# Kernel optimization log

Hardware: AMD Instinct MI355X
Metric: run time of the kernel (lower is better)

The kernel has to match this reference:

```python
import jax, jax.numpy as jnp
import numpy as np

IN_C, DIM, OUT_C, N_PIECES = 3, 256, 256, 20
BATCH, SET_N = 16, 128


def _xavier(k, shape, fan_in, fan_out):
    limit = float(np.sqrt(6.0 / (fan_in + fan_out)))
    return jax.random.uniform(k, shape, jnp.float32, -limit, limit)


def setup_inputs() -> dict:
    key = jax.random.key(0)
    ks = jax.random.split(key, 9)
    return {
        "x": jax.random.normal(ks[0], (BATCH, IN_C, SET_N), jnp.float32),
        "conv1_w": _xavier(ks[1], (DIM, IN_C), IN_C, DIM),
        "conv1_b": jnp.zeros((DIM,), jnp.float32),
        "conv2_w": _xavier(ks[2], (DIM, DIM), DIM, DIM),
        "conv2_b": jnp.zeros((DIM,), jnp.float32),
        "pool_w": jax.random.normal(ks[3], (DIM, N_PIECES + 1), jnp.float32) * 0.1,
        "lin1_w": _xavier(ks[4], (DIM, DIM), DIM, DIM),
        "lin1_b": jnp.zeros((DIM,), jnp.float32),
        "lin2_w": _xavier(ks[5], (OUT_C, DIM), DIM, OUT_C),
        "lin2_b": jnp.zeros((OUT_C,), jnp.float32),
        "cls1_w": _xavier(ks[6], (OUT_C, OUT_C), OUT_C, OUT_C),
        "cls1_b": jnp.zeros((OUT_C,), jnp.float32),
        "cls2_w": _xavier(ks[7], (10, OUT_C), OUT_C, 10),
        "cls2_b": jnp.zeros((10,), jnp.float32),
    }


def _fspool(x, pool_w, tau=1.0):
    # x: (B, C, N); pool_w: (C, N_PIECES+1). n is None -> full sets, mask is all ones.
    B, C, N = x.shape
    # piecewise-linear continuous weights evaluated at ratios i/(N-1)
    ratios = jnp.clip(jnp.arange(N, dtype=x.dtype) / max(N - 1, 1), 0.0, 1.0)  # (N,)
    idx_f = N_PIECES * ratios
    idx = jnp.floor(idx_f).astype(jnp.int32)
    frac = idx_f - idx.astype(x.dtype)
    left = pool_w[:, idx]                                   # (C, N)
    right = pool_w[:, jnp.clip(idx + 1, 0, N_PIECES)]       # (C, N)
    w = (1.0 - frac) * left + frac * right                  # (C, N)
    # relaxed continuous sort (NeuralSort / deterministic_sort), descending
    s = x.reshape(B * C, N, 1)
    A = jnp.abs(s - jnp.swapaxes(s, 1, 2))                  # (BC, N, N)
    Bsum = A.sum(axis=2, keepdims=True)                     # == A @ 1 1^T rowsums, (BC, N, 1)
    scaling = (N + 1 - 2 * (jnp.arange(N) + 1)).astype(x.dtype)  # (N,)
    Cmat = s * scaling[None, None, :]                       # (BC, N, N)
    P = jax.nn.softmax(jnp.swapaxes(Cmat - Bsum, 1, 2) / tau, axis=-1)  # (BC, N, N)
    xs = jnp.matmul(P, s).reshape(B, C, N)                  # soft-sorted, descending
    pooled = (xs * w[None]).sum(axis=2)                     # (B, C)
    return pooled, P


def reference(x, conv1_w, conv1_b, conv2_w, conv2_b, pool_w,
              lin1_w, lin1_b, lin2_w, lin2_b, cls1_w, cls1_b, cls2_w, cls2_b):
    # conv1x1 stack: (B, IN_C, N) -> (B, DIM, N)
    h = jnp.einsum('dc,bcn->bdn', conv1_w, x) + conv1_b[None, :, None]
    h = jax.nn.relu(h)
    h = jnp.einsum('dc,bcn->bdn', conv2_w, h) + conv2_b[None, :, None]
    pooled, _ = _fspool(h, pool_w)                          # (B, DIM)
    z = jax.nn.relu(pooled @ lin1_w.T + lin1_b)
    z = z @ lin2_w.T + lin2_b                               # (B, OUT_C)
    z = jax.nn.relu(z @ cls1_w.T + cls1_b)
    return z @ cls2_w.T + cls2_b                            # (B, 10)
```

## Files before the change

### kernel.cpp

```cpp
#include <hip/hip_runtime.h>
#include <math.h>


#if __has_builtin(__builtin_amdgcn_exp2f)
#define EXP2F(x) __builtin_amdgcn_exp2f(x)
#else
#define EXP2F(x) exp2f(x)
#endif

__global__ __launch_bounds__(256) void conv12_kernel(
    const float* __restrict__ x, const float* __restrict__ w1,
    const float* __restrict__ b1, const float* __restrict__ W2,
    const float* __restrict__ b2, float* __restrict__ H2)
{
    __shared__ float xs[3][64];
    __shared__ float As[16][16];
    __shared__ float Bs[16][64];

    int tid = threadIdx.x;
    int bx  = blockIdx.x;
    int d0  = blockIdx.y * 16;
    int b   = bx >> 1;
    int n0  = (bx & 1) * 64;

    if (tid < 192) {
        int c = tid >> 6, n = tid & 63;
        xs[c][n] = x[b * 384 + c * 128 + n0 + n];
    }
    __syncthreads();

    int tx = tid & 15, ty = tid >> 4;
    float acc[4] = {};

    for (int k0 = 0; k0 < 256; k0 += 16) {
        {
            int dl = tid & 15, kk = tid >> 4;
            As[kk][dl] = W2[(d0 + dl) * 256 + k0 + kk];
        }
        #pragma unroll
        for (int q = 0; q < 4; q++) {
            int idx = q * 256 + tid;
            int krel = idx >> 6, nl = idx & 63;
            int k = k0 + krel;
            float h = fmaf(w1[k * 3 + 0], xs[0][nl],
                      fmaf(w1[k * 3 + 1], xs[1][nl],
                      fmaf(w1[k * 3 + 2], xs[2][nl], b1[k])));
            Bs[krel][nl] = fmaxf(h, 0.0f);
        }
        __syncthreads();
        #pragma unroll
        for (int kk = 0; kk < 16; kk++) {
            float a  = As[kk][ty];
            float4 bv = *(const float4*)(&Bs[kk][tx * 4]);
            acc[0] = fmaf(a, bv.x, acc[0]);
            acc[1] = fmaf(a, bv.y, acc[1]);
            acc[2] = fmaf(a, bv.z, acc[2]);
            acc[3] = fmaf(a, bv.w, acc[3]);
        }
        __syncthreads();
    }

    int d = d0 + ty;
    float bias = b2[d];
    float4 o = make_float4(acc[0] + bias, acc[1] + bias,
                           acc[2] + bias, acc[3] + bias);
    *(float4*)(H2 + b * 32768 + d * 128 + n0 + tx * 4) = o;
}

__device__ __forceinline__ float pool_weight(const float* __restrict__ pw, int j)
{
    float ratio = (float)j / 127.0f;
    float idx_f = 20.0f * ratio;
    int idx = (int)idx_f;
    float frac = idx_f - (float)idx;
    int idx2 = idx + 1 > 20 ? 20 : idx + 1;
    return (1.0f - frac) * pw[idx] + frac * pw[idx2];
}

__global__ __launch_bounds__(256, 8) void fspool_kernel(
    const float* __restrict__ s_glob,
    const float* __restrict__ pool_w,
    float* __restrict__ pooled)
{
    const float LOG2E = 1.4426950408889634f;
    __shared__ float ss[2][128];
    __shared__ float bb[2][128];
    __shared__ float part[2][2];

    int tid  = threadIdx.x;
    int wave = tid >> 6;
    int rl   = wave >> 1;
    int half = wave & 1;
    int lane = tid & 63;
    int i    = half * 64 + lane;
    int row  = blockIdx.x * 2 + rl;

    float si = s_glob[row * 128 + i];
    ss[rl][i] = si;
    __syncthreads();

    float a0 = 0.f, a1 = 0.f, a2 = 0.f, a3 = 0.f;
    #pragma unroll 4
    for (int j = 0; j < 128; j += 4) {
        float4 sv = *(const float4*)(&ss[rl][j]);
        a0 += fabsf(si - sv.x);
        a1 += fabsf(si - sv.y);
        a2 += fabsf(si - sv.z);
        a3 += fabsf(si - sv.w);
    }
    bb[rl][i] = ((a0 + a1) + (a2 + a3)) * LOG2E;
    __syncthreads();

    float scal = (float)(127 - 2 * i) * LOG2E;
    float m0 = -1e30f, m1 = -1e30f, m2 = -1e30f, m3 = -1e30f;
    #pragma unroll 4
    for (int k = 0; k < 128; k += 4) {
        float4 sv = *(const float4*)(&ss[rl][k]);
        float4 bv = *(const float4*)(&bb[rl][k]);
        m0 = fmaxf(m0, fmaf(sv.x, scal, -bv.x));
        m1 = fmaxf(m1, fmaf(sv.y, scal, -bv.y));
        m2 = fmaxf(m2, fmaf(sv.z, scal, -bv.z));
        m3 = fmaxf(m3, fmaf(sv.w, scal, -bv.w));
    }
    float m = fmaxf(fmaxf(m0, m1), fmaxf(m2, m3));

    float se0 = 0.f, se1 = 0.f, se2 = 0.f, se3 = 0.f;
    float sd0 = 0.f, sd1 = 0.f, sd2 = 0.f, sd3 = 0.f;
    #pragma unroll 4
    for (int k = 0; k < 128; k += 4) {
        float4 sv = *(const float4*)(&ss[rl][k]);
        float4 bv = *(const float4*)(&bb[rl][k]);
        float e0 = EXP2F(fmaf(sv.x, scal, -bv.x) - m);
        float e1 = EXP2F(fmaf(sv.y, scal, -bv.y) - m);
        float e2 = EXP2F(fmaf(sv.z, scal, -bv.z) - m);
        float e3 = EXP2F(fmaf(sv.w, scal, -bv.w) - m);
        se0 += e0; se1 += e1; se2 += e2; se3 += e3;
        sd0 = fmaf(e0, sv.x, sd0);
        sd1 = fmaf(e1, sv.y, sd1);
        sd2 = fmaf(e2, sv.z, sd2);
        sd3 = fmaf(e3, sv.w, sd3);
    }
    float xs = ((sd0 + sd1) + (sd2 + sd3)) / ((se0 + se1) + (se2 + se3));

    int c = row & 255;
    float p = xs * pool_weight(pool_w + c * 21, i);
    #pragma unroll
    for (int off = 32; off > 0; off >>= 1)
        p += __shfl_xor(p, off);
    if (lane == 0) part[rl][half] = p;
    __syncthreads();
    if (tid < 2)
        pooled[blockIdx.x * 2 + tid] = part[tid][0] + part[tid][1];
}

__device__ __forceinline__ void dense1024(
    const float* __restrict__ W, const float* __restrict__ Bv,
    const float* in_lds, float* out_lds, int tid, bool do_relu)
{
    int o = tid >> 2, p = tid & 3;
    const float* wr = W + o * 256 + p * 64;
    const float* ir = in_lds + p * 64;
    float acc = 0.0f;
    #pragma unroll
    for (int k = 0; k < 64; k += 4) {
        float4 wv = *(const float4*)(wr + k);
        float4 iv = *(const float4*)(ir + k);
        acc = fmaf(wv.x, iv.x, acc);
        acc = fmaf(wv.y, iv.y, acc);
        acc = fmaf(wv.z, iv.z, acc);
        acc = fmaf(wv.w, iv.w, acc);
    }
    acc += __shfl_xor(acc, 1);
    acc += __shfl_xor(acc, 2);
    if (p == 0) {
        acc += Bv[o];
        out_lds[o] = do_relu ? fmaxf(acc, 0.0f) : acc;
    }
}

__global__ __launch_bounds__(1024) void tail_kernel(
    const float* __restrict__ pooled,
    const float* __restrict__ W1, const float* __restrict__ B1,
    const float* __restrict__ W2, const float* __restrict__ B2,
    const float* __restrict__ W3, const float* __restrict__ B3,
    const float* __restrict__ W4, const float* __restrict__ B4,
    float* __restrict__ out)
{
    __shared__ float za[256], zb[256];
    int b = blockIdx.x, tid = threadIdx.x;
    if (tid < 256) za[tid] = pooled[b * 256 + tid];
    __syncthreads();
    dense1024(W1, B1, za, zb, tid, true);
    __syncthreads();
    dense1024(W2, B2, zb, za, tid, false);
    __syncthreads();
    dense1024(W3, B3, za, zb, tid, true);
    __syncthreads();
    if (tid < 640) {
        int o = tid >> 6, kb = tid & 63;
        float4 wv = *(const float4*)(W4 + o * 256 + kb * 4);
        float4 zv = *(const float4*)(zb + kb * 4);
        float p = fmaf(wv.x, zv.x, fmaf(wv.y, zv.y,
                  fmaf(wv.z, zv.z, wv.w * zv.w)));
        #pragma unroll
        for (int off = 32; off > 0; off >>= 1)
            p += __shfl_xor(p, off);
        if (kb == 0) out[b * 10 + o] = p + B4[o];
    }
}

extern "C" void kernel_launch(void* const* d_in, const int* in_sizes, int n_in,
                              void* d_out, int out_size, void* d_ws, size_t ws_size,
                              hipStream_t stream)
{
    (void)in_sizes; (void)n_in; (void)out_size; (void)ws_size;
    const float* x       = (const float*)d_in[0];
    const float* conv1_w = (const float*)d_in[1];
    const float* conv1_b = (const float*)d_in[2];
    const float* conv2_w = (const float*)d_in[3];
    const float* conv2_b = (const float*)d_in[4];
    const float* pool_w  = (const float*)d_in[5];
    const float* lin1_w  = (const float*)d_in[6];
    const float* lin1_b  = (const float*)d_in[7];
    const float* lin2_w  = (const float*)d_in[8];
    const float* lin2_b  = (const float*)d_in[9];
    const float* cls1_w  = (const float*)d_in[10];
    const float* cls1_b  = (const float*)d_in[11];
    const float* cls2_w  = (const float*)d_in[12];
    const float* cls2_b  = (const float*)d_in[13];
    float* out = (float*)d_out;

    float* ws     = (float*)d_ws;
    float* H2     = ws;
    float* pooled = ws + 524288;

    conv12_kernel<<<dim3(32, 16), 256, 0, stream>>>(x, conv1_w, conv1_b,
                                                    conv2_w, conv2_b, H2);
    fspool_kernel<<<2048, 256, 0, stream>>>(H2, pool_w, pooled);
    tail_kernel<<<16, 1024, 0, stream>>>(pooled,
        lin1_w, lin1_b, lin2_w, lin2_b, cls1_w, cls1_b, cls2_w, cls2_b, out);
}
```

Baseline: 59.69 us.

## Process two sorted elements per thread with one wave per fspool row

Each wave now owns a whole 128-element row, and each lane handles two output positions. Every shared-memory load of s and B is therefore reused for two softmax rows. The s and B values are interleaved as float2 pairs, so one float4 LDS read covers two columns. The cross-wave partial-sum exchange and final block sync are gone, since each wave writes its pooled value directly. The grid is halved and there is more work per thread, which raises register pressure and gives fewer blocks for latency hiding.

```diff
diff --git a/kernel.cpp b/kernel.cpp
--- a/kernel.cpp
+++ b/kernel.cpp
@@ -77,80 +77,85 @@
     return (1.0f - frac) * pw[idx] + frac * pw[idx2];
 }
 
-__global__ __launch_bounds__(256, 8) void fspool_kernel(
+__global__ __launch_bounds__(256) void fspool_kernel(
     const float* __restrict__ s_glob,
     const float* __restrict__ pool_w,
     float* __restrict__ pooled)
 {
     const float LOG2E = 1.4426950408889634f;
-    __shared__ float ss[2][128];
-    __shared__ float bb[2][128];
-    __shared__ float part[2][2];
-
-    int tid  = threadIdx.x;
-    int wave = tid >> 6;
-    int rl   = wave >> 1;
-    int half = wave & 1;
-    int lane = tid & 63;
-    int i    = half * 64 + lane;
-    int row  = blockIdx.x * 2 + rl;
-
-    float si = s_glob[row * 128 + i];
-    ss[rl][i] = si;
-    __syncthreads();
-
+    __shared__ __align__(16) float  ss[4][128];
+    __shared__ __align__(16) float2 sb[4][128];
+
+    int tid = threadIdx.x;
+    int w   = tid >> 6;
+    int l   = tid & 63;
+    int row = blockIdx.x * 4 + w;
+
+    float2 sv = *(const float2*)(s_glob + row * 128 + l * 2);
+    *(float2*)(&ss[w][l * 2]) = sv;
+    __syncthreads();
+
+    float si0 = ss[w][l];
+    float si1 = ss[w][l + 64];
     float a0 = 0.f, a1 = 0.f, a2 = 0.f, a3 = 0.f;
+    float c0 = 0.f, c1 = 0.f, c2 = 0.f, c3 = 0.f;
     #pragma unroll 4
     for (int j = 0; j < 128; j += 4) {
-        float4 sv = *(const float4*)(&ss[rl][j]);
-        a0 += fabsf(si - sv.x);
-        a1 += fabsf(si - sv.y);
-        a2 += fabsf(si - sv.z);
-        a3 += fabsf(si - sv.w);
-    }
-    bb[rl][i] = ((a0 + a1) + (a2 + a3)) * LOG2E;
-    __syncthreads();
-
-    float scal = (float)(127 - 2 * i) * LOG2E;
-    float m0 = -1e30f, m1 = -1e30f, m2 = -1e30f, m3 = -1e30f;
+        float4 s4 = *(const float4*)(&ss[w][j]);
+        a0 += fabsf(si0 - s4.x);
+        a1 += fabsf(si0 - s4.y);
+        a2 += fabsf(si0 - s4.z);
+        a3 += fabsf(si0 - s4.w);
+        c0 += fabsf(si1 - s4.x);
+        c1 += fabsf(si1 - s4.y);
+        c2 += fabsf(si1 - s4.z);
+        c3 += fabsf(si1 - s4.w);
+    }
+    float B0 = ((a0 + a1) + (a2 + a3)) * LOG2E;
+    float B1 = ((c0 + c1) + (c2 + c3)) * LOG2E;
+    sb[w][l]      = make_float2(si0, B0);
+    sb[w][l + 64] = make_float2(si1, B1);
+    __syncthreads();
+
+    float scal0 = (float)(127 - 2 * l) * LOG2E;
+    float scal1 = (float)(127 - 2 * (l + 64)) * LOG2E;
+
+    float m00 = -1e30f, m01 = -1e30f, m10 = -1e30f, m11 = -1e30f;
     #pragma unroll 4
-    for (int k = 0; k < 128; k += 4) {
-        float4 sv = *(const float4*)(&ss[rl][k]);
-        float4 bv = *(const float4*)(&bb[rl][k]);
-        m0 = fmaxf(m0, fmaf(sv.x, scal, -bv.x));
-        m1 = fmaxf(m1, fmaf(sv.y, scal, -bv.y));
-        m2 = fmaxf(m2, fmaf(sv.z, scal, -bv.z));
-        m3 = fmaxf(m3, fmaf(sv.w, scal, -bv.w));
-    }
-    float m = fmaxf(fmaxf(m0, m1), fmaxf(m2, m3));
-
-    float se0 = 0.f, se1 = 0.f, se2 = 0.f, se3 = 0.f;
-    float sd0 = 0.f, sd1 = 0.f, sd2 = 0.f, sd3 = 0.f;
+    for (int i = 0; i < 128; i += 2) {
+        float4 p = *(const float4*)(&sb[w][i]);
+        m00 = fmaxf(m00, fmaf(p.x, scal0, -p.y));
+        m01 = fmaxf(m01, fmaf(p.z, scal0, -p.w));
+        m10 = fmaxf(m10, fmaf(p.x, scal1, -p.y));
+        m11 = fmaxf(m11, fmaf(p.z, scal1, -p.w));
+    }
+    float m0 = fmaxf(m00, m01), m1 = fmaxf(m10, m11);
+
+    float se0a = 0.f, se0b = 0.f, sd0a = 0.f, sd0b = 0.f;
+    float se1a = 0.f, se1b = 0.f, sd1a = 0.f, sd1b = 0.f;
     #pragma unroll 4
-    for (int k = 0; k < 128; k += 4) {
-        float4 sv = *(const float4*)(&ss[rl][k]);
-        float4 bv = *(const float4*)(&bb[rl][k]);
-        float e0 = EXP2F(fmaf(sv.x, scal, -bv.x) - m);
-        float e1 = EXP2F(fmaf(sv.y, scal, -bv.y) - m);
-        float e2 = EXP2F(fmaf(sv.z, scal, -bv.z) - m);
-        float e3 = EXP2F(fmaf(sv.w, scal, -bv.w) - m);
-        se0 += e0; se1 += e1; se2 += e2; se3 += e3;
-        sd0 = fmaf(e0, sv.x, sd0);
-        sd1 = fmaf(e1, sv.y, sd1);
-        sd2 = fmaf(e2, sv.z, sd2);
-        sd3 = fmaf(e3, sv.w, sd3);
-    }
-    float xs = ((sd0 + sd1) + (sd2 + sd3)) / ((se0 + se1) + (se2 + se3));
+    for (int i = 0; i < 128; i += 2) {
+        float4 p = *(const float4*)(&sb[w][i]);
+        float e0a = EXP2F(fmaf(p.x, scal0, -p.y) - m0);
+        float e0b = EXP2F(fmaf(p.z, scal0, -p.w) - m0);
+        float e1a = EXP2F(fmaf(p.x, scal1, -p.y) - m1);
+        float e1b = EXP2F(fmaf(p.z, scal1, -p.w) - m1);
+        se0a += e0a; sd0a = fmaf(e0a, p.x, sd0a);
+        se0b += e0b; sd0b = fmaf(e0b, p.z, sd0b);
+        se1a += e1a; sd1a = fmaf(e1a, p.x, sd1a);
+        se1b += e1b; sd1b = fmaf(e1b, p.z, sd1b);
+    }
+    float xs0 = (sd0a + sd0b) / (se0a + se0b);
+    float xs1 = (sd1a + sd1b) / (se1a + se1b);
 
     int c = row & 255;
-    float p = xs * pool_weight(pool_w + c * 21, i);
+    const float* pw = pool_w + c * 21;
+    float part = xs0 * pool_weight(pw, l) + xs1 * pool_weight(pw, l + 64);
+
     #pragma unroll
     for (int off = 32; off > 0; off >>= 1)
-        p += __shfl_xor(p, off);
-    if (lane == 0) part[rl][half] = p;
-    __syncthreads();
-    if (tid < 2)
-        pooled[blockIdx.x * 2 + tid] = part[tid][0] + part[tid][1];
+        part += __shfl_xor(part, off);
+    if (l == 0) pooled[row] = part;
 }
 
 __device__ __forceinline__ void dense1024(
@@ -236,7 +241,7 @@
 
     conv12_kernel<<<dim3(32, 16), 256, 0, stream>>>(x, conv1_w, conv1_b,
                                                     conv2_w, conv2_b, H2);
-    fspool_kernel<<<2048, 256, 0, stream>>>(H2, pool_w, pooled);
+    fspool_kernel<<<1024, 256, 0, stream>>>(H2, pool_w, pooled);
     tail_kernel<<<16, 1024, 0, stream>>>(pooled,
         lin1_w, lin1_b, lin2_w, lin2_b, cls1_w, cls1_b, cls2_w, cls2_b, out);
 }
```

Result: slower. 61.58 us (+3.2%).
